# Optimization experiments

Measured on AMD Instinct MI355X. Metric: run time of the kernel, lower is better.

## Reference

```python
import jax, jax.numpy as jnp
import numpy as np

V = 10000   # vocab_size
H = 512     # hidden_dim
D = 16      # max huffman path depth (pad length)
B = 8192    # batch


def setup_inputs() -> dict:
    key = jax.random.key(0)
    k1, k2, k3, k4, k5 = jax.random.split(key, 5)
    hidden = jax.random.normal(k1, (B, H), dtype=jnp.float32)
    target_words = jax.random.randint(k2, (B,), 0, V)
    # Batched per-word Linear(hidden_dim, path_len, bias=False) weights, padded to D rows.
    weights = jax.random.normal(k3, (V, D, H), dtype=jnp.float32) * 0.02
    # Binary huffman codes (BCE targets), padded to D; lengths are true path lengths.
    codes = jax.random.randint(k4, (V, D), 0, 2).astype(jnp.float32)
    lengths = jax.random.randint(k5, (V,), 8, D + 1)
    return {"hidden": hidden, "target_words": target_words,
            "weights": weights, "codes": codes, "lengths": lengths}


def reference(hidden, target_words, weights, codes, lengths):
    # Gather each sample's word-specific output layer, code, and path length.
    W = weights[target_words]          # [B, D, H]
    t = codes[target_words]            # [B, D]
    L = lengths[target_words]          # [B]
    # Per-sample tiny linear: logits over the huffman path nodes.
    logits = jnp.einsum('bdh,bh->bd', W, hidden)  # [B, D]
    # Stable BCE-with-logits: max(x,0) - x*t + log1p(exp(-|x|))
    bce = jnp.maximum(logits, 0.0) - logits * t + jnp.log1p(jnp.exp(-jnp.abs(logits)))
    mask = (jnp.arange(D)[None, :] < L[:, None]).astype(logits.dtype)  # [B, D]
    # F.binary_cross_entropy_with_logits default reduction='mean' over the path.
    per_word = jnp.sum(bce * mask, axis=1) / L.astype(logits.dtype)    # [B]
    # sum over batch / batch size
    return jnp.mean(per_word)
```

## Files before the change

### kernel.cpp

```cpp
#include <hip/hip_runtime.h>
#include <hip/hip_bf16.h>

#define BATCH 8192
#define HID   512
#define DEPTH 16

__global__ __launch_bounds__(256) void hsm_main_kernel(
    const float* __restrict__ hidden,
    const int*   __restrict__ target,
    const float* __restrict__ weights,
    const float* __restrict__ codes,
    const int*   __restrict__ lengths,
    float*       __restrict__ partial,
    float*       __restrict__ out_atomic)
{
    __shared__ float sh[HID];
    __shared__ float slog[DEPTH];

    const int b   = blockIdx.x;
    const int tid = threadIdx.x;
    const int w   = target[b];

    const float2* hrow = (const float2*)(hidden + (size_t)b * HID);
    ((float2*)sh)[tid] = hrow[tid];
    __syncthreads();

    const int wave = tid >> 6;
    const int lane = tid & 63;
    const float4* shv = (const float4*)sh;

#pragma unroll
    for (int di = 0; di < 4; ++di) {
        const int d = wave * 4 + di;
        const float4* wrow =
            (const float4*)(weights + ((size_t)w * DEPTH + d) * HID);
        float acc = 0.0f;
#pragma unroll
        for (int p = 0; p < 2; ++p) {
            const int idx = p * 64 + lane;
            float4 wv = wrow[idx];
            float4 hv = shv[idx];
            acc = fmaf(wv.x, hv.x, acc);
            acc = fmaf(wv.y, hv.y, acc);
            acc = fmaf(wv.z, hv.z, acc);
            acc = fmaf(wv.w, hv.w, acc);
        }
#pragma unroll
        for (int off = 32; off > 0; off >>= 1)
            acc += __shfl_down(acc, off, 64);
        if (lane == 0) slog[d] = acc;
    }
    __syncthreads();

    if (tid == 0) {
        const int L = lengths[w];
        const float* crow = codes + (size_t)w * DEPTH;
        float s = 0.0f;
#pragma unroll
        for (int d = 0; d < DEPTH; ++d) {
            if (d < L) {
                const float x = slog[d];
                const float t = crow[d];
                s += fmaxf(x, 0.0f) - x * t + log1pf(expf(-fabsf(x)));
            }
        }
        const float v = (s / (float)L) * (1.0f / (float)BATCH);
        if (partial) partial[b] = v;
        else         atomicAdd(out_atomic, v);
    }
}

__global__ __launch_bounds__(256) void hsm_reduce_kernel(
    const float* __restrict__ partial, float* __restrict__ out)
{
    __shared__ float sdata[256];
    float s = 0.0f;
    for (int i = threadIdx.x; i < BATCH; i += 256) s += partial[i];
    sdata[threadIdx.x] = s;
    __syncthreads();
#pragma unroll
    for (int stride = 128; stride > 0; stride >>= 1) {
        if (threadIdx.x < stride)
            sdata[threadIdx.x] += sdata[threadIdx.x + stride];
        __syncthreads();
    }
    if (threadIdx.x == 0) out[0] = sdata[0];
}

__global__ void hsm_zero_kernel(float* out) { out[0] = 0.0f; }

extern "C" void kernel_launch(void* const* d_in, const int* in_sizes, int n_in,
                              void* d_out, int out_size, void* d_ws, size_t ws_size,
                              hipStream_t stream)
{
    const float* hidden  = (const float*)d_in[0];
    const int*   target  = (const int*)  d_in[1];
    const float* weights = (const float*)d_in[2];
    const float* codes   = (const float*)d_in[3];
    const int*   lengths = (const int*)  d_in[4];
    float* out = (float*)d_out;

    if (ws_size >= BATCH * sizeof(float)) {
        float* partial = (float*)d_ws;
        hsm_main_kernel<<<BATCH, 256, 0, stream>>>(
            hidden, target, weights, codes, lengths, partial, nullptr);
        hsm_reduce_kernel<<<1, 256, 0, stream>>>(partial, out);
    } else {
        hsm_zero_kernel<<<1, 1, 0, stream>>>(out);
        hsm_main_kernel<<<BATCH, 256, 0, stream>>>(
            hidden, target, weights, codes, lengths, nullptr, out);
    }
}
```

Before: 437.0 us.

## Map one wavefront per sample and compute BCE lane-parallel without shared memory

Each 256-thread block now handles four samples, one per wavefront, instead of one sample per block. Each wave keeps its hidden row in registers and loops over all 16 path rows with butterfly xor reductions, so it no longer needs shared memory or block barriers. The BCE term is evaluated in parallel across lanes with fast __expf and summed with a 16-lane shuffle reduction. The atomic fallback is removed, so the kernel now always requires workspace for the partial sums. Each wave also does more serial reduction work per sample.

```diff
diff --git a/kernel.cpp b/kernel.cpp
--- a/kernel.cpp
+++ b/kernel.cpp
@@ -11,63 +11,54 @@
     const float* __restrict__ weights,
     const float* __restrict__ codes,
     const int*   __restrict__ lengths,
-    float*       __restrict__ partial,
-    float*       __restrict__ out_atomic)
+    float*       __restrict__ partial)
 {
-    __shared__ float sh[HID];
-    __shared__ float slog[DEPTH];
-
-    const int b   = blockIdx.x;
-    const int tid = threadIdx.x;
-    const int w   = target[b];
-
-    const float2* hrow = (const float2*)(hidden + (size_t)b * HID);
-    ((float2*)sh)[tid] = hrow[tid];
-    __syncthreads();
-
+    const int tid  = threadIdx.x;
     const int wave = tid >> 6;
     const int lane = tid & 63;
-    const float4* shv = (const float4*)sh;
+    const int b    = blockIdx.x * 4 + wave;
+    const int w    = target[b];
 
+    const float4* hrow = (const float4*)(hidden + (size_t)b * HID);
+    const float4 h0 = hrow[lane];
+    const float4 h1 = hrow[lane + 64];
+
+    const float4* wbase = (const float4*)(weights + (size_t)w * (DEPTH * HID));
+
+    float xmine = 0.0f;
+#pragma unroll 4
+    for (int d = 0; d < DEPTH; ++d) {
+        const float4* wrow = wbase + d * (HID / 4);
+        const float4 w0 = wrow[lane];
+        const float4 w1 = wrow[lane + 64];
+        float acc;
+        acc = w0.x * h0.x;
+        acc = fmaf(w0.y, h0.y, acc);
+        acc = fmaf(w0.z, h0.z, acc);
+        acc = fmaf(w0.w, h0.w, acc);
+        acc = fmaf(w1.x, h1.x, acc);
+        acc = fmaf(w1.y, h1.y, acc);
+        acc = fmaf(w1.z, h1.z, acc);
+        acc = fmaf(w1.w, h1.w, acc);
 #pragma unroll
-    for (int di = 0; di < 4; ++di) {
-        const int d = wave * 4 + di;
-        const float4* wrow =
-            (const float4*)(weights + ((size_t)w * DEPTH + d) * HID);
-        float acc = 0.0f;
+        for (int m = 32; m >= 1; m >>= 1)
+            acc += __shfl_xor(acc, m, 64);
+        xmine = (lane == d) ? acc : xmine;
+    }
+
+    const int L = lengths[w];
+    float v = 0.0f;
+    if (lane < DEPTH && lane < L) {
+        const float t = codes[(size_t)w * DEPTH + lane];
+        const float x = xmine;
+        v = fmaxf(x, 0.0f) - x * t + log1pf(__expf(-fabsf(x)));
+    }
 #pragma unroll
-        for (int p = 0; p < 2; ++p) {
-            const int idx = p * 64 + lane;
-            float4 wv = wrow[idx];
-            float4 hv = shv[idx];
-            acc = fmaf(wv.x, hv.x, acc);
-            acc = fmaf(wv.y, hv.y, acc);
-            acc = fmaf(wv.z, hv.z, acc);
-            acc = fmaf(wv.w, hv.w, acc);
-        }
-#pragma unroll
-        for (int off = 32; off > 0; off >>= 1)
-            acc += __shfl_down(acc, off, 64);
-        if (lane == 0) slog[d] = acc;
-    }
-    __syncthreads();
+    for (int m = 8; m >= 1; m >>= 1)
+        v += __shfl_xor(v, m, 64);
 
-    if (tid == 0) {
-        const int L = lengths[w];
-        const float* crow = codes + (size_t)w * DEPTH;
-        float s = 0.0f;
-#pragma unroll
-        for (int d = 0; d < DEPTH; ++d) {
-            if (d < L) {
-                const float x = slog[d];
-                const float t = crow[d];
-                s += fmaxf(x, 0.0f) - x * t + log1pf(expf(-fabsf(x)));
-            }
-        }
-        const float v = (s / (float)L) * (1.0f / (float)BATCH);
-        if (partial) partial[b] = v;
-        else         atomicAdd(out_atomic, v);
-    }
+    if (lane == 0)
+        partial[b] = v / ((float)L * (float)BATCH);
 }
 
 __global__ __launch_bounds__(256) void hsm_reduce_kernel(
@@ -87,8 +78,6 @@
     if (threadIdx.x == 0) out[0] = sdata[0];
 }
 
-__global__ void hsm_zero_kernel(float* out) { out[0] = 0.0f; }
-
 extern "C" void kernel_launch(void* const* d_in, const int* in_sizes, int n_in,
                               void* d_out, int out_size, void* d_ws, size_t ws_size,
                               hipStream_t stream)
@@ -99,15 +88,9 @@
     const float* codes   = (const float*)d_in[3];
     const int*   lengths = (const int*)  d_in[4];
     float* out = (float*)d_out;
+    float* partial = (float*)d_ws;
 
-    if (ws_size >= BATCH * sizeof(float)) {
-        float* partial = (float*)d_ws;
-        hsm_main_kernel<<<BATCH, 256, 0, stream>>>(
-            hidden, target, weights, codes, lengths, partial, nullptr);
-        hsm_reduce_kernel<<<1, 256, 0, stream>>>(partial, out);
-    } else {
-        hsm_zero_kernel<<<1, 1, 0, stream>>>(out);
-        hsm_main_kernel<<<BATCH, 256, 0, stream>>>(
-            hidden, target, weights, codes, lengths, nullptr, out);
-    }
+    hsm_main_kernel<<<BATCH / 4, 256, 0, stream>>>(
+        hidden, target, weights, codes, lengths, partial);
+    hsm_reduce_kernel<<<1, 256, 0, stream>>>(partial, out);
 }
```

New measurement: 425.6 us. 2.6% less time.
